# Kernel tuning notes

Measured on AMD Instinct MI355X. Metric: run time of the kernel, lower is better.

The kernel has to match this reference:

```python
import jax, jax.numpy as jnp
import numpy as np

H, W = 256, 256
N_PIXELS = H * W
MAX_DIST = float(np.sqrt(H ** 2 + W ** 2))
RESIZED = jnp.array([H, W], dtype=jnp.float32)

# all_img_locations: cartesian product of rows x cols, shape [N_PIXELS, 2] as (row, col)
_rr, _cc = jnp.meshgrid(jnp.arange(H), jnp.arange(W), indexing='ij')
LOCS = jnp.stack([_rr, _cc], axis=-1).reshape(-1, 2).astype(jnp.float32)


def setup_inputs() -> dict:
    key = jax.random.key(0)
    k1, k2, k3 = jax.random.split(key, 3)
    B, M = 8, 128
    # probability map in open interval (0,1) so log(p) and log(1-p) are finite
    prob_map = jnp.clip(jax.random.uniform(k1, (B, H, W), dtype=jnp.float32), 1e-4, 1.0 - 1e-4)
    # gt heatmap: mostly <1 with a sprinkling of exact 1.0 'center' pixels (so pos_count > 0)
    u = jax.random.uniform(k2, (B, H, W), dtype=jnp.float32)
    gt_map = jnp.where(u > 0.999, jnp.float32(1.0), u * 0.999)
    # ground-truth points (row, col) in [0, H) x [0, W)
    gt = jax.random.uniform(k3, (B, M, 2), dtype=jnp.float32) * RESIZED
    # original image sizes (height, width)
    orig_sizes = jnp.ones((B, 2), dtype=jnp.float32) * 1024.0
    return {"prob_map": prob_map, "gt_map": gt_map, "gt": gt, "orig_sizes": orig_sizes}


def _center_focal_loss(pred, g, alpha=2, beta=4):
    pos = (g == 1.0).astype(pred.dtype)
    neg = (g < 1.0).astype(pred.dtype)
    pos_term = (1.0 - pred) ** alpha * jnp.log(pred) * pos
    neg_term = (1.0 - g) ** beta * pred ** alpha * jnp.log1p(-pred) * neg
    return -((pos_term + neg_term).sum() / pos.sum())


def _whd_terms(pm_b, gt_b, orig_size_b):
    norm = orig_size_b / RESIZED                      # [2]
    nx = LOCS * norm                                  # [N, 2]
    ny = gt_b * norm                                  # [M, 2]
    diff = nx[:, None, :] - ny[None, :, :]            # [N, M, 2]
    d = jnp.sqrt(jnp.sum(diff * diff, axis=-1))       # [N, M]
    p = pm_b.reshape(-1)                              # [N]
    n_est = p.sum()
    term1 = jnp.sum(p * d.min(axis=1)) / (n_est + 1e-6)
    weighted = (1.0 - p)[:, None] * MAX_DIST + p[:, None] * d
    term2 = weighted.min(axis=0).mean()               # generalized mean reduces to min over pixels
    return term1, term2


def reference(prob_map, gt_map, gt, orig_sizes):
    terms_1, terms_2 = jax.vmap(_whd_terms)(prob_map, gt, orig_sizes)
    # original loop overwrites terms_3 each iteration -> only last batch element's focal loss survives
    terms_3 = _center_focal_loss(prob_map[-1], gt_map[-1])
    return terms_1.mean() + terms_2.mean() + terms_3
```

## Files before the change

kernel.cpp:

```cpp
#include <hip/hip_runtime.h>
#include <hip/hip_bf16.h>
#include <math.h>


#define HH 256
#define WW 256
#define NPIX (HH*WW)
#define MM 128
#define BB 8
#define MAXDIST 362.03867196751236f
#define PBLK 64
#define TPB 256
#define PXT 4
#define MCH 16
#define NCH (MM/MCH)

#if defined(__has_builtin)
#if __has_builtin(__builtin_amdgcn_sqrtf)
#define FSQRT(x) __builtin_amdgcn_sqrtf(x)
#else
#define FSQRT(x) sqrtf(x)
#endif
#else
#define FSQRT(x) sqrtf(x)
#endif

__device__ __forceinline__ float wave_sum(float v) {
#pragma unroll
  for (int off = 32; off > 0; off >>= 1) v += __shfl_xor(v, off, 64);
  return v;
}

__global__ __launch_bounds__(TPB) void whd_init(unsigned int* __restrict__ colmin) {
  int i = blockIdx.x * TPB + threadIdx.x;
  if (i < BB * MM) colmin[i] = 0x7F800000u;
}

__global__ __launch_bounds__(TPB) void whd_main(
    const float* __restrict__ prob, const float* __restrict__ gtmap,
    const float* __restrict__ gt, const float* __restrict__ osz,
    unsigned int* __restrict__ colmin, float* __restrict__ partials) {
  const int b   = blockIdx.x / PBLK;
  const int blk = blockIdx.x % PBLK;
  const int tid = threadIdx.x;

  __shared__ float2 sgt[MM];
  __shared__ float wred[TPB / 64][4];

  const float ny = osz[b * 2 + 0] * (1.0f / HH);
  const float nx = osz[b * 2 + 1] * (1.0f / WW);

  if (tid < MM) {
    float gy = gt[(b * MM + tid) * 2 + 0] * ny;
    float gx = gt[(b * MM + tid) * 2 + 1] * nx;
    sgt[tid] = make_float2(gy, gx);
  }
  __syncthreads();

  const int pixBase = blk * (NPIX / PBLK) + tid * PXT;
  const float pyf = (float)(pixBase >> 8) * ny;
  const int col0 = pixBase & (WW - 1);

  const float* pp = prob + b * NPIX + pixBase;
  float4 pv = *(const float4*)(pp);
  float p[PXT] = {pv.x, pv.y, pv.z, pv.w};

  float pxf[PXT], bb[PXT], md[PXT];
#pragma unroll
  for (int i = 0; i < PXT; i++) {
    pxf[i] = (float)(col0 + i) * nx;
    bb[i]  = (1.0f - p[i]) * MAXDIST;
    md[i]  = 3.0e38f;
  }

  const int lane = tid & 63;

#pragma unroll 1
  for (int c = 0; c < NCH; c++) {
    float gx[MCH], dy2[MCH], cm[MCH];
#pragma unroll
    for (int j = 0; j < MCH; j++) {
      float2 g = sgt[c * MCH + j];
      float dy = pyf - g.x;
      dy2[j] = dy * dy;
      gx[j]  = g.y;
      cm[j]  = 3.0e38f;
    }
#pragma unroll
    for (int i = 0; i < PXT; i++) {
      const float pi = p[i], bi = bb[i], xi = pxf[i];
      float mdi = md[i];
#pragma unroll
      for (int j = 0; j < MCH; j++) {
        float dx = xi - gx[j];
        float d  = FSQRT(fmaf(dx, dx, dy2[j]));
        mdi   = fminf(mdi, d);
        cm[j] = fminf(cm[j], fmaf(pi, d, bi));
      }
      md[i] = mdi;
    }

    {
      const bool hi5 = (lane & 32) != 0;
#pragma unroll
      for (int k = 0; k < 8; k++) {
        float keep = hi5 ? cm[k + 8] : cm[k];
        float send = hi5 ? cm[k] : cm[k + 8];
        cm[k] = fminf(keep, __shfl_xor(send, 32, 64));
      }
      const bool hi4 = (lane & 16) != 0;
#pragma unroll
      for (int k = 0; k < 4; k++) {
        float keep = hi4 ? cm[k + 4] : cm[k];
        float send = hi4 ? cm[k] : cm[k + 4];
        cm[k] = fminf(keep, __shfl_xor(send, 16, 64));
      }
      const bool hi3 = (lane & 8) != 0;
#pragma unroll
      for (int k = 0; k < 2; k++) {
        float keep = hi3 ? cm[k + 2] : cm[k];
        float send = hi3 ? cm[k] : cm[k + 2];
        cm[k] = fminf(keep, __shfl_xor(send, 8, 64));
      }
      const bool hi2 = (lane & 4) != 0;
      {
        float keep = hi2 ? cm[1] : cm[0];
        float send = hi2 ? cm[0] : cm[1];
        cm[0] = fminf(keep, __shfl_xor(send, 4, 64));
      }
      float v = cm[0];
      v = fminf(v, __shfl_xor(v, 1, 64));
      v = fminf(v, __shfl_xor(v, 2, 64));
      if ((lane & 3) == 0)
        atomicMin(&colmin[b * MM + c * MCH + (lane >> 2)], __float_as_uint(v));
    }
  }

  float spd = 0.0f, sp = 0.0f;
#pragma unroll
  for (int i = 0; i < PXT; i++) {
    spd = fmaf(p[i], md[i], spd);
    sp += p[i];
  }

  float fs = 0.0f, fc = 0.0f;
  if (b == BB - 1) {
    const float* gp = gtmap + b * NPIX + pixBase;
    float4 gv4 = *(const float4*)(gp);
    float gv[PXT] = {gv4.x, gv4.y, gv4.z, gv4.w};
#pragma unroll
    for (int i = 0; i < PXT; i++) {
      float g = gv[i], pi = p[i];
      if (g == 1.0f) {
        float om = 1.0f - pi;
        fs += om * om * logf(pi);
        fc += 1.0f;
      } else {
        float t = 1.0f - g, t2 = t * t;
        fs += t2 * t2 * pi * pi * log1pf(-pi);
      }
    }
  }

  spd = wave_sum(spd);
  sp  = wave_sum(sp);
  fs  = wave_sum(fs);
  fc  = wave_sum(fc);

  const int wid = tid >> 6;
  if (lane == 0) {
    wred[wid][0] = spd; wred[wid][1] = sp; wred[wid][2] = fs; wred[wid][3] = fc;
  }
  __syncthreads();
  if (tid == 0) {
    float a = 0, c2 = 0, e = 0, f = 0;
#pragma unroll
    for (int w = 0; w < TPB / 64; w++) {
      a += wred[w][0]; c2 += wred[w][1]; e += wred[w][2]; f += wred[w][3];
    }
    float* pt = partials + blockIdx.x * 4;
    pt[0] = a; pt[1] = c2; pt[2] = e; pt[3] = f;
  }
}

__global__ __launch_bounds__(TPB) void whd_final(const unsigned int* __restrict__ colmin,
                                                 const float* __restrict__ partials,
                                                 float* __restrict__ out) {
  __shared__ float sh[TPB];
  const int tid = threadIdx.x;

  float s = 0.0f;
  for (int i = tid; i < BB * MM; i += TPB) s += __uint_as_float(colmin[i]);
  sh[tid] = s;
  __syncthreads();
  for (int st = TPB / 2; st > 0; st >>= 1) {
    if (tid < st) sh[tid] += sh[tid + st];
    __syncthreads();
  }
  const float t2m = sh[0] * (1.0f / (BB * MM));
  __syncthreads();

  if (tid < BB) {
    float a = 0.0f, c = 0.0f;
    for (int i = 0; i < PBLK; i++) {
      const float* pt = partials + (tid * PBLK + i) * 4;
      a += pt[0];
      c += pt[1];
    }
    sh[tid] = a / (c + 1e-6f);
  }
  __syncthreads();

  if (tid == 0) {
    float t1 = 0.0f;
    for (int b2 = 0; b2 < BB; b2++) t1 += sh[b2];
    t1 *= (1.0f / BB);
    float fsum = 0.0f, fcnt = 0.0f;
    for (int i = (BB - 1) * PBLK; i < BB * PBLK; i++) {
      fsum += partials[i * 4 + 2];
      fcnt += partials[i * 4 + 3];
    }
    out[0] = t1 + t2m - fsum / fcnt;
  }
}

extern "C" void kernel_launch(void* const* d_in, const int* in_sizes, int n_in,
                              void* d_out, int out_size, void* d_ws, size_t ws_size,
                              hipStream_t stream) {
  const float* prob  = (const float*)d_in[0];
  const float* gtmap = (const float*)d_in[1];
  const float* gt    = (const float*)d_in[2];
  const float* osz   = (const float*)d_in[3];
  float* out = (float*)d_out;

  unsigned int* colmin = (unsigned int*)d_ws;
  float* partials = (float*)((char*)d_ws + 4096);

  whd_init<<<(BB * MM + TPB - 1) / TPB, TPB, 0, stream>>>(colmin);
  whd_main<<<BB * PBLK, TPB, 0, stream>>>(prob, gtmap, gt, osz, colmin, partials);
  whd_final<<<1, TPB, 0, stream>>>(colmin, partials, out);
}
```

Baseline: 87.01 us.

## Replace global atomics with per-block LDS column mins and drop init kernel

Column minima are now reduced into shared memory with LDS atomics, and each block writes its own per-block column-min vector to workspace. The final kernel reduces these across blocks, so the separate init kernel launch and the global atomicMin contention go away. The grid is doubled and each thread handles 2 pixels instead of 4, which gives more blocks for occupancy but less reuse of each gt load. The final reduction now reads 1024x128 floats instead of 1024, in a single block.

After: 92.68 us. 6.5% more time.

```diff
diff --git a/kernel.cpp b/kernel.cpp
--- a/kernel.cpp
+++ b/kernel.cpp
@@ -1,5 +1,4 @@
 #include <hip/hip_runtime.h>
-#include <hip/hip_bf16.h>
 #include <math.h>
 
 
@@ -9,9 +8,10 @@
 #define MM 128
 #define BB 8
 #define MAXDIST 362.03867196751236f
-#define PBLK 64
+#define PBLK 128
+#define NBLK (BB*PBLK)
 #define TPB 256
-#define PXT 4
+#define PXT 2
 #define MCH 16
 #define NCH (MM/MCH)
 
@@ -31,20 +31,17 @@
   return v;
 }
 
-__global__ __launch_bounds__(TPB) void whd_init(unsigned int* __restrict__ colmin) {
-  int i = blockIdx.x * TPB + threadIdx.x;
-  if (i < BB * MM) colmin[i] = 0x7F800000u;
-}
-
 __global__ __launch_bounds__(TPB) void whd_main(
     const float* __restrict__ prob, const float* __restrict__ gtmap,
     const float* __restrict__ gt, const float* __restrict__ osz,
-    unsigned int* __restrict__ colmin, float* __restrict__ partials) {
-  const int b   = blockIdx.x / PBLK;
-  const int blk = blockIdx.x % PBLK;
+    float* __restrict__ partials, float* __restrict__ colminblk) {
+  const int b   = blockIdx.x >> 7;
+  const int blk = blockIdx.x & (PBLK - 1);
   const int tid = threadIdx.x;
+  const int lane = tid & 63;
 
   __shared__ float2 sgt[MM];
+  __shared__ unsigned scm[MM];
   __shared__ float wred[TPB / 64][4];
 
   const float ny = osz[b * 2 + 0] * (1.0f / HH);
@@ -54,6 +51,7 @@
     float gy = gt[(b * MM + tid) * 2 + 0] * ny;
     float gx = gt[(b * MM + tid) * 2 + 1] * nx;
     sgt[tid] = make_float2(gy, gx);
+    scm[tid] = 0x7F800000u;
   }
   __syncthreads();
 
@@ -62,8 +60,8 @@
   const int col0 = pixBase & (WW - 1);
 
   const float* pp = prob + b * NPIX + pixBase;
-  float4 pv = *(const float4*)(pp);
-  float p[PXT] = {pv.x, pv.y, pv.z, pv.w};
+  float2 pv = *(const float2*)(pp);
+  float p[PXT] = {pv.x, pv.y};
 
   float pxf[PXT], bb[PXT], md[PXT];
 #pragma unroll
@@ -72,8 +70,6 @@
     bb[i]  = (1.0f - p[i]) * MAXDIST;
     md[i]  = 3.0e38f;
   }
-
-  const int lane = tid & 63;
 
 #pragma unroll 1
   for (int c = 0; c < NCH; c++) {
@@ -132,7 +128,7 @@
       v = fminf(v, __shfl_xor(v, 1, 64));
       v = fminf(v, __shfl_xor(v, 2, 64));
       if ((lane & 3) == 0)
-        atomicMin(&colmin[b * MM + c * MCH + (lane >> 2)], __float_as_uint(v));
+        atomicMin(&scm[c * MCH + (lane >> 2)], __float_as_uint(v));
     }
   }
 
@@ -146,8 +142,8 @@
   float fs = 0.0f, fc = 0.0f;
   if (b == BB - 1) {
     const float* gp = gtmap + b * NPIX + pixBase;
-    float4 gv4 = *(const float4*)(gp);
-    float gv[PXT] = {gv4.x, gv4.y, gv4.z, gv4.w};
+    float2 gv2 = *(const float2*)(gp);
+    float gv[PXT] = {gv2.x, gv2.y};
 #pragma unroll
     for (int i = 0; i < PXT; i++) {
       float g = gv[i], pi = p[i];
@@ -172,6 +168,9 @@
     wred[wid][0] = spd; wred[wid][1] = sp; wred[wid][2] = fs; wred[wid][3] = fc;
   }
   __syncthreads();
+
+  if (tid < MM)
+    colminblk[blockIdx.x * MM + tid] = __uint_as_float(scm[tid]);
   if (tid == 0) {
     float a = 0, c2 = 0, e = 0, f = 0;
 #pragma unroll
@@ -183,44 +182,50 @@
   }
 }
 
-__global__ __launch_bounds__(TPB) void whd_final(const unsigned int* __restrict__ colmin,
+__global__ __launch_bounds__(TPB) void whd_final(const float* __restrict__ colminblk,
                                                  const float* __restrict__ partials,
                                                  float* __restrict__ out) {
-  __shared__ float sh[TPB];
   const int tid = threadIdx.x;
-
-  float s = 0.0f;
-  for (int i = tid; i < BB * MM; i += TPB) s += __uint_as_float(colmin[i]);
-  sh[tid] = s;
+  __shared__ float sT[TPB / 64];
+  __shared__ float sA[BB], sC[BB], sF[BB], sG[BB];
+
+  const int m  = tid & (MM - 1);
+  const int b0 = tid >> 7;
+  float mn0 = 3.0e38f, mn1 = 3.0e38f, mn2 = 3.0e38f, mn3 = 3.0e38f;
+#pragma unroll 4
+  for (int k = 0; k < PBLK; k++) {
+    mn0 = fminf(mn0, colminblk[((b0 + 0) * PBLK + k) * MM + m]);
+    mn1 = fminf(mn1, colminblk[((b0 + 2) * PBLK + k) * MM + m]);
+    mn2 = fminf(mn2, colminblk[((b0 + 4) * PBLK + k) * MM + m]);
+    mn3 = fminf(mn3, colminblk[((b0 + 6) * PBLK + k) * MM + m]);
+  }
+  float smin = (mn0 + mn1) + (mn2 + mn3);
+  smin = wave_sum(smin);
+  if ((tid & 63) == 0) sT[tid >> 6] = smin;
+
+  const int g = tid >> 5;
+  const int i = tid & 31;
+  float a = 0, c = 0, e = 0, f = 0;
+  for (int k = i; k < PBLK; k += 32) {
+    const float* pt = partials + (g * PBLK + k) * 4;
+    a += pt[0]; c += pt[1]; e += pt[2]; f += pt[3];
+  }
+#pragma unroll
+  for (int off = 16; off > 0; off >>= 1) {
+    a += __shfl_xor(a, off, 64); c += __shfl_xor(c, off, 64);
+    e += __shfl_xor(e, off, 64); f += __shfl_xor(f, off, 64);
+  }
+  if (i == 0) { sA[g] = a; sC[g] = c; sF[g] = e; sG[g] = f; }
   __syncthreads();
-  for (int st = TPB / 2; st > 0; st >>= 1) {
-    if (tid < st) sh[tid] += sh[tid + st];
-    __syncthreads();
-  }
-  const float t2m = sh[0] * (1.0f / (BB * MM));
-  __syncthreads();
-
-  if (tid < BB) {
-    float a = 0.0f, c = 0.0f;
-    for (int i = 0; i < PBLK; i++) {
-      const float* pt = partials + (tid * PBLK + i) * 4;
-      a += pt[0];
-      c += pt[1];
-    }
-    sh[tid] = a / (c + 1e-6f);
-  }
-  __syncthreads();
 
   if (tid == 0) {
+    float t2 = (sT[0] + sT[1] + sT[2] + sT[3]) * (1.0f / (BB * MM));
     float t1 = 0.0f;
-    for (int b2 = 0; b2 < BB; b2++) t1 += sh[b2];
+    for (int b2 = 0; b2 < BB; b2++) t1 += sA[b2] / (sC[b2] + 1e-6f);
     t1 *= (1.0f / BB);
     float fsum = 0.0f, fcnt = 0.0f;
-    for (int i = (BB - 1) * PBLK; i < BB * PBLK; i++) {
-      fsum += partials[i * 4 + 2];
-      fcnt += partials[i * 4 + 3];
-    }
-    out[0] = t1 + t2m - fsum / fcnt;
+    for (int b2 = 0; b2 < BB; b2++) { fsum += sF[b2]; fcnt += sG[b2]; }
+    out[0] = t1 + t2 - fsum / fcnt;
   }
 }
 
@@ -233,10 +238,9 @@
   const float* osz   = (const float*)d_in[3];
   float* out = (float*)d_out;
 
-  unsigned int* colmin = (unsigned int*)d_ws;
-  float* partials = (float*)((char*)d_ws + 4096);
-
-  whd_init<<<(BB * MM + TPB - 1) / TPB, TPB, 0, stream>>>(colmin);
-  whd_main<<<BB * PBLK, TPB, 0, stream>>>(prob, gtmap, gt, osz, colmin, partials);
-  whd_final<<<1, TPB, 0, stream>>>(colmin, partials, out);
-}
+  float* partials  = (float*)d_ws;
+  float* colminblk = (float*)((char*)d_ws + NBLK * 16);
+
+  whd_main<<<NBLK, TPB, 0, stream>>>(prob, gtmap, gt, osz, partials, colminblk);
+  whd_final<<<1, TPB, 0, stream>>>(colminblk, partials, out);
+}
```
